# Performance work log

Hardware: AMD Instinct MI355X
Metric: run time of the kernel (lower is better)

The kernel has to match this reference:

```python
import jax, jax.numpy as jnp
import numpy as np

STEPS = 96
H = 4096
I = 1024


def setup_inputs() -> dict:
    key = jax.random.key(0)
    ks = jax.random.split(key, 12)
    kI = 1.0 / np.sqrt(H)  # torch RNN/Linear default init bound
    u = lambda k, shape, b: jax.random.uniform(k, shape, jnp.float32, -b, b)
    return {
        "x": jax.random.normal(ks[0], (1, 1, I), jnp.float32),
        "W_ih0": u(ks[1], (H, I), kI),
        "b_ih0": u(ks[2], (H,), kI),
        "W_hh0": u(ks[3], (H, H), kI),
        "b_hh0": u(ks[4], (H,), kI),
        "W_ih1": u(ks[5], (H, H), kI),
        "b_ih1": u(ks[6], (H,), kI),
        "W_hh1": u(ks[7], (H, H), kI),
        "b_hh1": u(ks[8], (H,), kI),
        "W_fc": u(ks[9], (1, H), kI),
        "b_fc": u(ks[10], (1,), kI),
    }


def reference(x, W_ih0, b_ih0, W_hh0, b_hh0, W_ih1, b_ih1, W_hh1, b_hh1, W_fc, b_fc):
    # x: (1, 1, I) -- seq=batch=1 (the only shapes the torch module accepts).
    xv = x[0, 0]  # (I,) sliding feature window
    h_init = jnp.zeros((2, H), x.dtype)  # num_layers=2 hidden state

    def step(carry, _):
        xw, h = carry
        h0 = jnp.tanh(W_ih0 @ xw + b_ih0 + W_hh0 @ h[0] + b_hh0)
        h1 = jnp.tanh(W_ih1 @ h0 + b_ih1 + W_hh1 @ h[1] + b_hh1)
        y = W_fc @ h1 + b_fc  # (1,) scalar prediction
        xw_new = jnp.concatenate([xw[1:], y])  # shift window, append prediction
        # torch: h0.detach() each outer iteration -> cut grad through carried state
        h_new = jax.lax.stop_gradient(jnp.stack([h0, h1]))
        return (xw_new, h_new), y

    _, ys = jax.lax.scan(step, (xv, h_init), None, length=STEPS)  # ys: (96, 1)
    return ys.reshape(1, STEPS, 1)
```

## Files before the change

kernel.cpp:

```cpp
#include <hip/hip_runtime.h>

#define STEPS 96
#define HDIM 4096
#define IDIM 1024
#define BLOCKS 256
#define THREADS 1024
#define WAVES (THREADS / 64)
#define ROWS_PER_BLOCK (HDIM / BLOCKS)

__device__ inline void wload8(const unsigned short* __restrict__ w, float* o) {
  uint4 u = *reinterpret_cast<const uint4*>(w);
  o[0] = __uint_as_float(u.x << 16);
  o[1] = __uint_as_float(u.x & 0xffff0000u);
  o[2] = __uint_as_float(u.y << 16);
  o[3] = __uint_as_float(u.y & 0xffff0000u);
  o[4] = __uint_as_float(u.z << 16);
  o[5] = __uint_as_float(u.z & 0xffff0000u);
  o[6] = __uint_as_float(u.w << 16);
  o[7] = __uint_as_float(u.w & 0xffff0000u);
}
__device__ inline void wload8(const float* __restrict__ w, float* o) {
  float4 a = *reinterpret_cast<const float4*>(w);
  float4 b = *reinterpret_cast<const float4*>(w + 4);
  o[0] = a.x; o[1] = a.y; o[2] = a.z; o[3] = a.w;
  o[4] = b.x; o[5] = b.y; o[6] = b.z; o[7] = b.w;
}
__device__ inline void wload4(const unsigned short* __restrict__ w, float* o) {
  uint2 u = *reinterpret_cast<const uint2*>(w);
  o[0] = __uint_as_float(u.x << 16);
  o[1] = __uint_as_float(u.x & 0xffff0000u);
  o[2] = __uint_as_float(u.y << 16);
  o[3] = __uint_as_float(u.y & 0xffff0000u);
}
__device__ inline void wload4(const float* __restrict__ w, float* o) {
  float4 f = *reinterpret_cast<const float4*>(w);
  o[0] = f.x; o[1] = f.y; o[2] = f.z; o[3] = f.w;
}

template <typename WT, int NC>
__device__ inline float dot_gh(const WT* __restrict__ w, const float* __restrict__ v, int lane) {
  float acc = 0.f;
#pragma unroll
  for (int it = 0; it < NC / 512; ++it) {
    const int base = it * 512 + lane * 8;
    float wf[8];
    wload8(w + base, wf);
    float4 a = *reinterpret_cast<const float4*>(v + base);
    float4 b = *reinterpret_cast<const float4*>(v + base + 4);
    acc += wf[0] * a.x + wf[1] * a.y + wf[2] * a.z + wf[3] * a.w +
           wf[4] * b.x + wf[5] * b.y + wf[6] * b.z + wf[7] * b.w;
  }
  return acc;
}

template <typename WT>
__device__ inline float dot_win(const WT* __restrict__ w, const float* v, int lane) {
  float acc = 0.f;
#pragma unroll
  for (int it = 0; it < IDIM / 512; ++it) {
    const int base = it * 512 + lane * 8;
    float wf[8];
    wload8(w + base, wf);
#pragma unroll
    for (int k = 0; k < 8; ++k) acc += wf[k] * v[base + k];
  }
  return acc;
}

__device__ inline float wave_reduce(float v) {
#pragma unroll
  for (int off = 32; off > 0; off >>= 1) v += __shfl_xor(v, off);
  return v;
}

template <typename WT>
struct Params {
  const WT *Wih0, *Whh0, *Wih1, *Whh1, *Wfc;
  const float *x, *b_ih0, *b_hh0, *b_ih1, *b_hh1, *b_fc;
  float* h0buf;
  float* h1buf;
  unsigned* leaf;
  unsigned* root;
  unsigned* flag;
  float* out;
};

template <typename WT>
__device__ inline void grid_barrier(const Params<WT>& p, unsigned gen) {
  __syncthreads();
  if (threadIdx.x == 0) {
    __threadfence();
    const int g = blockIdx.x & 7;
    unsigned prev = __hip_atomic_fetch_add(p.leaf + g * 32, 1u, __ATOMIC_RELAXED,
                                           __HIP_MEMORY_SCOPE_AGENT);
    if (prev == gen * (BLOCKS / 8) - 1) {
      unsigned r = __hip_atomic_fetch_add(p.root, 1u, __ATOMIC_RELAXED,
                                          __HIP_MEMORY_SCOPE_AGENT);
      if (r == gen * 8 - 1) {
        __hip_atomic_store(p.flag, gen, __ATOMIC_RELEASE, __HIP_MEMORY_SCOPE_AGENT);
      }
    }
    while (__hip_atomic_load(p.flag, __ATOMIC_RELAXED, __HIP_MEMORY_SCOPE_AGENT) < gen) {
      __builtin_amdgcn_s_sleep(1);
    }
    __threadfence();
  }
  __syncthreads();
}

template <typename WT>
__global__ void __launch_bounds__(THREADS, 4) rnn_kernel(Params<WT> p) {
  __shared__ float win[IDIM + STEPS];
  __shared__ float red[WAVES];

  const int tid = threadIdx.x;
  const int lane = tid & 63;
  const int wv = tid >> 6;
  const int blk = blockIdx.x;
  const int row = blk * ROWS_PER_BLOCK + wv;

  for (int i = tid; i < IDIM; i += THREADS) win[i] = p.x[i];
  __syncthreads();

  unsigned gen = 0;
  for (int t = 0; t < STEPS; ++t) {
    const int par = t & 1;
    float* h0n = p.h0buf + par * HDIM;
    const float* h0o = p.h0buf + (par ^ 1) * HDIM;
    float* h1n = p.h1buf + par * HDIM;
    const float* h1o = p.h1buf + (par ^ 1) * HDIM;

    {
      float acc = dot_win(p.Wih0 + (size_t)row * IDIM, win + t, lane) +
                  dot_gh<WT, HDIM>(p.Whh0 + (size_t)row * HDIM, h0o, lane);
      acc = wave_reduce(acc);
      if (lane == 0) h0n[row] = tanhf(acc + p.b_ih0[row] + p.b_hh0[row]);
    }
    grid_barrier(p, ++gen);

    {
      float acc = dot_gh<WT, HDIM>(p.Wih1 + (size_t)row * HDIM, h0n, lane) +
                  dot_gh<WT, HDIM>(p.Whh1 + (size_t)row * HDIM, h1o, lane);
      acc = wave_reduce(acc);
      if (lane == 0) h1n[row] = tanhf(acc + p.b_ih1[row] + p.b_hh1[row]);
    }
    grid_barrier(p, ++gen);

    {
      const int base = tid * 4;
      float wf[4];
      wload4(p.Wfc + base, wf);
      float4 h = *reinterpret_cast<const float4*>(h1n + base);
      float part = wf[0] * h.x + wf[1] * h.y + wf[2] * h.z + wf[3] * h.w;
      part = wave_reduce(part);
      if (lane == 0) red[wv] = part;
    }
    __syncthreads();
    if (tid == 0) {
      float y = p.b_fc[0];
#pragma unroll
      for (int i = 0; i < WAVES; ++i) y += red[i];
      win[IDIM + t] = y;
      if (blk == 0) p.out[t] = y;
    }
    __syncthreads();
  }
}

__device__ inline unsigned short f2bf(float f) {
  unsigned int u = __float_as_uint(f);
  u += 0x7fffu + ((u >> 16) & 1u);
  return (unsigned short)(u >> 16);
}

__global__ void cvt_kernel(const float* __restrict__ in, unsigned short* __restrict__ out, int n4) {
  int i = blockIdx.x * blockDim.x + threadIdx.x;
  const int stride = gridDim.x * blockDim.x;
  for (; i < n4; i += stride) {
    float4 f = reinterpret_cast<const float4*>(in)[i];
    ushort4 o;
    o.x = f2bf(f.x); o.y = f2bf(f.y); o.z = f2bf(f.z); o.w = f2bf(f.w);
    reinterpret_cast<ushort4*>(out)[i] = o;
  }
}

extern "C" void kernel_launch(void* const* d_in, const int* in_sizes, int n_in,
                              void* d_out, int out_size, void* d_ws, size_t ws_size,
                              hipStream_t stream) {
  const float* x = (const float*)d_in[0];
  const float* Wih0 = (const float*)d_in[1];
  const float* bih0 = (const float*)d_in[2];
  const float* Whh0 = (const float*)d_in[3];
  const float* bhh0 = (const float*)d_in[4];
  const float* Wih1 = (const float*)d_in[5];
  const float* bih1 = (const float*)d_in[6];
  const float* Whh1 = (const float*)d_in[7];
  const float* bhh1 = (const float*)d_in[8];
  const float* Wfc = (const float*)d_in[9];
  const float* bfc = (const float*)d_in[10];
  float* out = (float*)d_out;

  const size_t nIh0 = (size_t)HDIM * IDIM;
  const size_t nHh = (size_t)HDIM * HDIM;
  const size_t nFc = HDIM;
  const size_t bfBytes = (nIh0 + 3 * nHh + nFc) * 2;
  const size_t hFloats = 4 * (size_t)HDIM;
  const size_t barU32 = 8 * 32 + 32 + 32;
  const size_t dynBytes = hFloats * 4 + barU32 * 4;

  if (ws_size >= bfBytes + dynBytes + 256) {
    unsigned short* wih0 = (unsigned short*)d_ws;
    unsigned short* whh0 = wih0 + nIh0;
    unsigned short* wih1 = whh0 + nHh;
    unsigned short* whh1 = wih1 + nHh;
    unsigned short* wfc = whh1 + nHh;
    char* dyn = (char*)d_ws + ((bfBytes + 255) & ~(size_t)255);
    float* hbuf = (float*)dyn;
    unsigned* bar = (unsigned*)(dyn + hFloats * 4);

    cvt_kernel<<<4096, 256, 0, stream>>>(Wih0, wih0, (int)(nIh0 / 4));
    cvt_kernel<<<8192, 256, 0, stream>>>(Whh0, whh0, (int)(nHh / 4));
    cvt_kernel<<<8192, 256, 0, stream>>>(Wih1, wih1, (int)(nHh / 4));
    cvt_kernel<<<8192, 256, 0, stream>>>(Whh1, whh1, (int)(nHh / 4));
    cvt_kernel<<<8, 128, 0, stream>>>(Wfc, wfc, (int)(nFc / 4));
    hipMemsetAsync(dyn, 0, dynBytes, stream);

    Params<unsigned short> p;
    p.Wih0 = wih0; p.Whh0 = whh0; p.Wih1 = wih1; p.Whh1 = whh1; p.Wfc = wfc;
    p.x = x; p.b_ih0 = bih0; p.b_hh0 = bhh0; p.b_ih1 = bih1; p.b_hh1 = bhh1; p.b_fc = bfc;
    p.h0buf = hbuf; p.h1buf = hbuf + 2 * HDIM;
    p.leaf = bar; p.root = bar + 8 * 32; p.flag = bar + 8 * 32 + 32;
    p.out = out;

    void* args[] = {&p};
    hipLaunchCooperativeKernel(reinterpret_cast<void*>(&rnn_kernel<unsigned short>),
                               dim3(BLOCKS), dim3(THREADS), args, 0, stream);
  } else {
    char* dyn = (char*)d_ws;
    float* hbuf = (float*)dyn;
    unsigned* bar = (unsigned*)(dyn + hFloats * 4);
    hipMemsetAsync(dyn, 0, dynBytes, stream);

    Params<float> p;
    p.Wih0 = Wih0; p.Whh0 = Whh0; p.Wih1 = Wih1; p.Whh1 = Whh1; p.Wfc = Wfc;
    p.x = x; p.b_ih0 = bih0; p.b_hh0 = bhh0; p.b_ih1 = bih1; p.b_hh1 = bhh1; p.b_fc = bfc;
    p.h0buf = hbuf; p.h1buf = hbuf + 2 * HDIM;
    p.leaf = bar; p.root = bar + 8 * 32; p.flag = bar + 8 * 32 + 32;
    p.out = out;

    void* args[] = {&p};
    hipLaunchCooperativeKernel(reinterpret_cast<void*>(&rnn_kernel<float>),
                               dim3(BLOCKS), dim3(THREADS), args, 0, stream);
  }
}
```

Baseline: 3.924 ms.

## Keep bf16 weights resident in registers and LDS, reorder recurrence phases

Removes the separate bf16 conversion kernels and instead packs each block's weight rows into bf16 once at kernel start. Whh0, Wih1, Wih0 and Wfc slices are held in registers and the block's Whh1 rows in LDS, so the 96 steps no longer stream weights from HBM/L2. The phases are reordered so that the Whh1·h1 product runs before the barrier, and the Whh0·h0 product for the next step is fused with the Wih1·h0 pass. This reduces per-step memory traffic and keeps two grid barriers per step, with single h buffers. In exchange it uses very high register and LDS pressure (512 threads, 2 rows per wave), which may cause spills or limit occupancy, and it relies on careful ordering so that the single-buffered h0/h1 are safe.

Result: slower. 6.703 ms (+70.8%).

```diff
diff --git a/kernel.cpp b/kernel.cpp
--- a/kernel.cpp
+++ b/kernel.cpp
@@ -4,68 +4,20 @@
 #define HDIM 4096
 #define IDIM 1024
 #define BLOCKS 256
-#define THREADS 1024
-#define WAVES (THREADS / 64)
-#define ROWS_PER_BLOCK (HDIM / BLOCKS)
-
-__device__ inline void wload8(const unsigned short* __restrict__ w, float* o) {
-  uint4 u = *reinterpret_cast<const uint4*>(w);
-  o[0] = __uint_as_float(u.x << 16);
-  o[1] = __uint_as_float(u.x & 0xffff0000u);
-  o[2] = __uint_as_float(u.y << 16);
-  o[3] = __uint_as_float(u.y & 0xffff0000u);
-  o[4] = __uint_as_float(u.z << 16);
-  o[5] = __uint_as_float(u.z & 0xffff0000u);
-  o[6] = __uint_as_float(u.w << 16);
-  o[7] = __uint_as_float(u.w & 0xffff0000u);
-}
-__device__ inline void wload8(const float* __restrict__ w, float* o) {
-  float4 a = *reinterpret_cast<const float4*>(w);
-  float4 b = *reinterpret_cast<const float4*>(w + 4);
-  o[0] = a.x; o[1] = a.y; o[2] = a.z; o[3] = a.w;
-  o[4] = b.x; o[5] = b.y; o[6] = b.z; o[7] = b.w;
-}
-__device__ inline void wload4(const unsigned short* __restrict__ w, float* o) {
-  uint2 u = *reinterpret_cast<const uint2*>(w);
-  o[0] = __uint_as_float(u.x << 16);
-  o[1] = __uint_as_float(u.x & 0xffff0000u);
-  o[2] = __uint_as_float(u.y << 16);
-  o[3] = __uint_as_float(u.y & 0xffff0000u);
-}
-__device__ inline void wload4(const float* __restrict__ w, float* o) {
-  float4 f = *reinterpret_cast<const float4*>(w);
-  o[0] = f.x; o[1] = f.y; o[2] = f.z; o[3] = f.w;
-}
-
-template <typename WT, int NC>
-__device__ inline float dot_gh(const WT* __restrict__ w, const float* __restrict__ v, int lane) {
-  float acc = 0.f;
-#pragma unroll
-  for (int it = 0; it < NC / 512; ++it) {
-    const int base = it * 512 + lane * 8;
-    float wf[8];
-    wload8(w + base, wf);
-    float4 a = *reinterpret_cast<const float4*>(v + base);
-    float4 b = *reinterpret_cast<const float4*>(v + base + 4);
-    acc += wf[0] * a.x + wf[1] * a.y + wf[2] * a.z + wf[3] * a.w +
-           wf[4] * b.x + wf[5] * b.y + wf[6] * b.z + wf[7] * b.w;
-  }
-  return acc;
-}
-
-template <typename WT>
-__device__ inline float dot_win(const WT* __restrict__ w, const float* v, int lane) {
-  float acc = 0.f;
-#pragma unroll
-  for (int it = 0; it < IDIM / 512; ++it) {
-    const int base = it * 512 + lane * 8;
-    float wf[8];
-    wload8(w + base, wf);
-#pragma unroll
-    for (int k = 0; k < 8; ++k) acc += wf[k] * v[base + k];
-  }
-  return acc;
-}
+#define THREADS 512
+#define WAVES 8
+#define ROWS_PER_BLOCK 16
+
+__device__ inline unsigned short f2bf(float f) {
+  unsigned u = __float_as_uint(f);
+  u += 0x7fffu + ((u >> 16) & 1u);
+  return (unsigned short)(u >> 16);
+}
+__device__ inline unsigned pack2(float a, float b) {
+  return (unsigned)f2bf(a) | ((unsigned)f2bf(b) << 16);
+}
+__device__ inline float blo(unsigned p) { return __uint_as_float(p << 16); }
+__device__ inline float bhi(unsigned p) { return __uint_as_float(p & 0xffff0000u); }
 
 __device__ inline float wave_reduce(float v) {
 #pragma unroll
@@ -73,20 +25,14 @@
   return v;
 }
 
-template <typename WT>
 struct Params {
-  const WT *Wih0, *Whh0, *Wih1, *Whh1, *Wfc;
-  const float *x, *b_ih0, *b_hh0, *b_ih1, *b_hh1, *b_fc;
-  float* h0buf;
-  float* h1buf;
-  unsigned* leaf;
-  unsigned* root;
-  unsigned* flag;
-  float* out;
+  const float *x, *Wih0, *bih0, *Whh0, *bhh0, *Wih1, *bih1, *Whh1, *bhh1, *Wfc, *bfc;
+  float *h0, *h1;
+  unsigned *leaf, *root, *flag;
+  float *out;
 };
 
-template <typename WT>
-__device__ inline void grid_barrier(const Params<WT>& p, unsigned gen) {
+__device__ inline void grid_barrier(const Params& p, unsigned gen) {
   __syncthreads();
   if (threadIdx.x == 0) {
     __threadfence();
@@ -108,56 +54,132 @@
   __syncthreads();
 }
 
-template <typename WT>
-__global__ void __launch_bounds__(THREADS, 4) rnn_kernel(Params<WT> p) {
+__global__ void __launch_bounds__(THREADS, 2) rnn_kernel(Params p) {
+  __shared__ unsigned whh1[ROWS_PER_BLOCK * (HDIM / 2)];
   __shared__ float win[IDIM + STEPS];
   __shared__ float red[WAVES];
 
-  const int tid = threadIdx.x;
-  const int lane = tid & 63;
-  const int wv = tid >> 6;
-  const int blk = blockIdx.x;
-  const int row = blk * ROWS_PER_BLOCK + wv;
-
+  const int tid = threadIdx.x, lane = tid & 63, wv = tid >> 6, blk = blockIdx.x;
+  const int r0 = blk * ROWS_PER_BLOCK + wv * 2;
+  const int r1 = r0 + 1;
+
+  for (int rr = 0; rr < ROWS_PER_BLOCK; ++rr) {
+    const float* src = p.Whh1 + (size_t)(blk * ROWS_PER_BLOCK + rr) * HDIM;
+    for (int u = tid; u < HDIM / 2; u += THREADS) {
+      float2 f = *reinterpret_cast<const float2*>(src + 2 * u);
+      whh1[rr * (HDIM / 2) + u] = pack2(f.x, f.y);
+    }
+  }
   for (int i = tid; i < IDIM; i += THREADS) win[i] = p.x[i];
+
+  unsigned wA_ih0[8], wB_ih0[8];
+#pragma unroll
+  for (int j = 0; j < 8; ++j) {
+    const float* s0 = p.Wih0 + (size_t)r0 * IDIM + j * 128 + lane;
+    const float* s1 = p.Wih0 + (size_t)r1 * IDIM + j * 128 + lane;
+    wA_ih0[j] = pack2(s0[0], s0[64]);
+    wB_ih0[j] = pack2(s1[0], s1[64]);
+  }
+  unsigned wA_hh0[32], wB_hh0[32], wA_ih1[32], wB_ih1[32];
+#pragma unroll
+  for (int j = 0; j < 16; ++j) {
+    float4 f;
+    f = *reinterpret_cast<const float4*>(p.Whh0 + (size_t)r0 * HDIM + j * 256 + lane * 4);
+    wA_hh0[2 * j] = pack2(f.x, f.y); wA_hh0[2 * j + 1] = pack2(f.z, f.w);
+    f = *reinterpret_cast<const float4*>(p.Whh0 + (size_t)r1 * HDIM + j * 256 + lane * 4);
+    wB_hh0[2 * j] = pack2(f.x, f.y); wB_hh0[2 * j + 1] = pack2(f.z, f.w);
+    f = *reinterpret_cast<const float4*>(p.Wih1 + (size_t)r0 * HDIM + j * 256 + lane * 4);
+    wA_ih1[2 * j] = pack2(f.x, f.y); wA_ih1[2 * j + 1] = pack2(f.z, f.w);
+    f = *reinterpret_cast<const float4*>(p.Wih1 + (size_t)r1 * HDIM + j * 256 + lane * 4);
+    wB_ih1[2 * j] = pack2(f.x, f.y); wB_ih1[2 * j + 1] = pack2(f.z, f.w);
+  }
+  unsigned wfcp[4];
+  {
+    float4 f = *reinterpret_cast<const float4*>(p.Wfc + tid * 8);
+    wfcp[0] = pack2(f.x, f.y); wfcp[1] = pack2(f.z, f.w);
+    f = *reinterpret_cast<const float4*>(p.Wfc + tid * 8 + 4);
+    wfcp[2] = pack2(f.x, f.y); wfcp[3] = pack2(f.z, f.w);
+  }
+  const float bias0a = p.bih0[r0] + p.bhh0[r0];
+  const float bias0b = p.bih0[r1] + p.bhh0[r1];
+  const float bias1a = p.bih1[r0] + p.bhh1[r0];
+  const float bias1b = p.bih1[r1] + p.bhh1[r1];
+  const float bfc = p.bfc[0];
+
   __syncthreads();
 
+  float p1a = 0.f, p1b = 0.f;
   unsigned gen = 0;
+
   for (int t = 0; t < STEPS; ++t) {
-    const int par = t & 1;
-    float* h0n = p.h0buf + par * HDIM;
-    const float* h0o = p.h0buf + (par ^ 1) * HDIM;
-    float* h1n = p.h1buf + par * HDIM;
-    const float* h1o = p.h1buf + (par ^ 1) * HDIM;
-
+    float a1 = p1a, b1 = p1b;
+#pragma unroll
+    for (int j = 0; j < 8; ++j) {
+      float v0 = win[t + j * 128 + lane];
+      float v1 = win[t + j * 128 + 64 + lane];
+      a1 += v0 * blo(wA_ih0[j]) + v1 * bhi(wA_ih0[j]);
+      b1 += v0 * blo(wB_ih0[j]) + v1 * bhi(wB_ih0[j]);
+    }
+    a1 = wave_reduce(a1);
+    b1 = wave_reduce(b1);
+    if (lane == 0) {
+      p.h0[r0] = tanhf(a1 + bias0a);
+      p.h0[r1] = tanhf(b1 + bias0b);
+    }
+
+    float a2 = 0.f, b2 = 0.f;
     {
-      float acc = dot_win(p.Wih0 + (size_t)row * IDIM, win + t, lane) +
-                  dot_gh<WT, HDIM>(p.Whh0 + (size_t)row * HDIM, h0o, lane);
-      acc = wave_reduce(acc);
-      if (lane == 0) h0n[row] = tanhf(acc + p.b_ih0[row] + p.b_hh0[row]);
-    }
+      const unsigned* wl0 = whh1 + (wv * 2) * (HDIM / 2);
+      const unsigned* wl1 = wl0 + (HDIM / 2);
+#pragma unroll
+      for (int j = 0; j < 16; ++j) {
+        float4 v = *reinterpret_cast<const float4*>(p.h1 + j * 256 + lane * 4);
+        unsigned c0 = wl0[j * 128 + lane * 2], c1 = wl0[j * 128 + lane * 2 + 1];
+        unsigned d0 = wl1[j * 128 + lane * 2], d1 = wl1[j * 128 + lane * 2 + 1];
+        a2 += v.x * blo(c0) + v.y * bhi(c0) + v.z * blo(c1) + v.w * bhi(c1);
+        b2 += v.x * blo(d0) + v.y * bhi(d0) + v.z * blo(d1) + v.w * bhi(d1);
+      }
+    }
+
     grid_barrier(p, ++gen);
 
+    float q1a = 0.f, q1b = 0.f;
+#pragma unroll
+    for (int j = 0; j < 16; ++j) {
+      float4 v = *reinterpret_cast<const float4*>(p.h0 + j * 256 + lane * 4);
+      a2 += v.x * blo(wA_ih1[2 * j]) + v.y * bhi(wA_ih1[2 * j]) +
+            v.z * blo(wA_ih1[2 * j + 1]) + v.w * bhi(wA_ih1[2 * j + 1]);
+      b2 += v.x * blo(wB_ih1[2 * j]) + v.y * bhi(wB_ih1[2 * j]) +
+            v.z * blo(wB_ih1[2 * j + 1]) + v.w * bhi(wB_ih1[2 * j + 1]);
+      q1a += v.x * blo(wA_hh0[2 * j]) + v.y * bhi(wA_hh0[2 * j]) +
+             v.z * blo(wA_hh0[2 * j + 1]) + v.w * bhi(wA_hh0[2 * j + 1]);
+      q1b += v.x * blo(wB_hh0[2 * j]) + v.y * bhi(wB_hh0[2 * j]) +
+             v.z * blo(wB_hh0[2 * j + 1]) + v.w * bhi(wB_hh0[2 * j + 1]);
+    }
+    a2 = wave_reduce(a2);
+    b2 = wave_reduce(b2);
+    if (lane == 0) {
+      p.h1[r0] = tanhf(a2 + bias1a);
+      p.h1[r1] = tanhf(b2 + bias1b);
+    }
+    p1a = q1a;
+    p1b = q1b;
+
+    grid_barrier(p, ++gen);
+
     {
-      float acc = dot_gh<WT, HDIM>(p.Wih1 + (size_t)row * HDIM, h0n, lane) +
-                  dot_gh<WT, HDIM>(p.Whh1 + (size_t)row * HDIM, h1o, lane);
-      acc = wave_reduce(acc);
-      if (lane == 0) h1n[row] = tanhf(acc + p.b_ih1[row] + p.b_hh1[row]);
-    }
-    grid_barrier(p, ++gen);
-
-    {
-      const int base = tid * 4;
-      float wf[4];
-      wload4(p.Wfc + base, wf);
-      float4 h = *reinterpret_cast<const float4*>(h1n + base);
-      float part = wf[0] * h.x + wf[1] * h.y + wf[2] * h.z + wf[3] * h.w;
+      float4 v0 = *reinterpret_cast<const float4*>(p.h1 + tid * 8);
+      float4 v1 = *reinterpret_cast<const float4*>(p.h1 + tid * 8 + 4);
+      float part = v0.x * blo(wfcp[0]) + v0.y * bhi(wfcp[0]) +
+                   v0.z * blo(wfcp[1]) + v0.w * bhi(wfcp[1]) +
+                   v1.x * blo(wfcp[2]) + v1.y * bhi(wfcp[2]) +
+                   v1.z * blo(wfcp[3]) + v1.w * bhi(wfcp[3]);
       part = wave_reduce(part);
       if (lane == 0) red[wv] = part;
     }
     __syncthreads();
     if (tid == 0) {
-      float y = p.b_fc[0];
+      float y = bfc;
 #pragma unroll
       for (int i = 0; i < WAVES; ++i) y += red[i];
       win[IDIM + t] = y;
@@ -167,89 +189,35 @@
   }
 }
 
-__device__ inline unsigned short f2bf(float f) {
-  unsigned int u = __float_as_uint(f);
-  u += 0x7fffu + ((u >> 16) & 1u);
-  return (unsigned short)(u >> 16);
-}
-
-__global__ void cvt_kernel(const float* __restrict__ in, unsigned short* __restrict__ out, int n4) {
-  int i = blockIdx.x * blockDim.x + threadIdx.x;
-  const int stride = gridDim.x * blockDim.x;
-  for (; i < n4; i += stride) {
-    float4 f = reinterpret_cast<const float4*>(in)[i];
-    ushort4 o;
-    o.x = f2bf(f.x); o.y = f2bf(f.y); o.z = f2bf(f.z); o.w = f2bf(f.w);
-    reinterpret_cast<ushort4*>(out)[i] = o;
-  }
-}
-
 extern "C" void kernel_launch(void* const* d_in, const int* in_sizes, int n_in,
                               void* d_out, int out_size, void* d_ws, size_t ws_size,
                               hipStream_t stream) {
-  const float* x = (const float*)d_in[0];
-  const float* Wih0 = (const float*)d_in[1];
-  const float* bih0 = (const float*)d_in[2];
-  const float* Whh0 = (const float*)d_in[3];
-  const float* bhh0 = (const float*)d_in[4];
-  const float* Wih1 = (const float*)d_in[5];
-  const float* bih1 = (const float*)d_in[6];
-  const float* Whh1 = (const float*)d_in[7];
-  const float* bhh1 = (const float*)d_in[8];
-  const float* Wfc = (const float*)d_in[9];
-  const float* bfc = (const float*)d_in[10];
-  float* out = (float*)d_out;
-
-  const size_t nIh0 = (size_t)HDIM * IDIM;
-  const size_t nHh = (size_t)HDIM * HDIM;
-  const size_t nFc = HDIM;
-  const size_t bfBytes = (nIh0 + 3 * nHh + nFc) * 2;
-  const size_t hFloats = 4 * (size_t)HDIM;
-  const size_t barU32 = 8 * 32 + 32 + 32;
-  const size_t dynBytes = hFloats * 4 + barU32 * 4;
-
-  if (ws_size >= bfBytes + dynBytes + 256) {
-    unsigned short* wih0 = (unsigned short*)d_ws;
-    unsigned short* whh0 = wih0 + nIh0;
-    unsigned short* wih1 = whh0 + nHh;
-    unsigned short* whh1 = wih1 + nHh;
-    unsigned short* wfc = whh1 + nHh;
-    char* dyn = (char*)d_ws + ((bfBytes + 255) & ~(size_t)255);
-    float* hbuf = (float*)dyn;
-    unsigned* bar = (unsigned*)(dyn + hFloats * 4);
-
-    cvt_kernel<<<4096, 256, 0, stream>>>(Wih0, wih0, (int)(nIh0 / 4));
-    cvt_kernel<<<8192, 256, 0, stream>>>(Whh0, whh0, (int)(nHh / 4));
-    cvt_kernel<<<8192, 256, 0, stream>>>(Wih1, wih1, (int)(nHh / 4));
-    cvt_kernel<<<8192, 256, 0, stream>>>(Whh1, whh1, (int)(nHh / 4));
-    cvt_kernel<<<8, 128, 0, stream>>>(Wfc, wfc, (int)(nFc / 4));
-    hipMemsetAsync(dyn, 0, dynBytes, stream);
-
-    Params<unsigned short> p;
-    p.Wih0 = wih0; p.Whh0 = whh0; p.Wih1 = wih1; p.Whh1 = whh1; p.Wfc = wfc;
-    p.x = x; p.b_ih0 = bih0; p.b_hh0 = bhh0; p.b_ih1 = bih1; p.b_hh1 = bhh1; p.b_fc = bfc;
-    p.h0buf = hbuf; p.h1buf = hbuf + 2 * HDIM;
-    p.leaf = bar; p.root = bar + 8 * 32; p.flag = bar + 8 * 32 + 32;
-    p.out = out;
-
-    void* args[] = {&p};
-    hipLaunchCooperativeKernel(reinterpret_cast<void*>(&rnn_kernel<unsigned short>),
-                               dim3(BLOCKS), dim3(THREADS), args, 0, stream);
-  } else {
-    char* dyn = (char*)d_ws;
-    float* hbuf = (float*)dyn;
-    unsigned* bar = (unsigned*)(dyn + hFloats * 4);
-    hipMemsetAsync(dyn, 0, dynBytes, stream);
-
-    Params<float> p;
-    p.Wih0 = Wih0; p.Whh0 = Whh0; p.Wih1 = Wih1; p.Whh1 = Whh1; p.Wfc = Wfc;
-    p.x = x; p.b_ih0 = bih0; p.b_hh0 = bhh0; p.b_ih1 = bih1; p.b_hh1 = bhh1; p.b_fc = bfc;
-    p.h0buf = hbuf; p.h1buf = hbuf + 2 * HDIM;
-    p.leaf = bar; p.root = bar + 8 * 32; p.flag = bar + 8 * 32 + 32;
-    p.out = out;
-
-    void* args[] = {&p};
-    hipLaunchCooperativeKernel(reinterpret_cast<void*>(&rnn_kernel<float>),
-                               dim3(BLOCKS), dim3(THREADS), args, 0, stream);
-  }
-}
+  Params p;
+  p.x = (const float*)d_in[0];
+  p.Wih0 = (const float*)d_in[1];
+  p.bih0 = (const float*)d_in[2];
+  p.Whh0 = (const float*)d_in[3];
+  p.bhh0 = (const float*)d_in[4];
+  p.Wih1 = (const float*)d_in[5];
+  p.bih1 = (const float*)d_in[6];
+  p.Whh1 = (const float*)d_in[7];
+  p.bhh1 = (const float*)d_in[8];
+  p.Wfc = (const float*)d_in[9];
+  p.bfc = (const float*)d_in[10];
+  p.out = (float*)d_out;
+
+  float* hbuf = (float*)d_ws;
+  p.h0 = hbuf;
+  p.h1 = hbuf + HDIM;
+  unsigned* bar = (unsigned*)(hbuf + 2 * HDIM);
+  p.leaf = bar;
+  p.root = bar + 8 * 32;
+  p.flag = bar + 8 * 32 + 32;
+
+  const size_t dynBytes = 2 * HDIM * sizeof(float) + (8 * 32 + 64) * sizeof(unsigned);
+  hipMemsetAsync(d_ws, 0, dynBytes, stream);
+
+  void* args[] = {&p};
+  hipLaunchCooperativeKernel(reinterpret_cast<void*>(&rnn_kernel),
+                             dim3(BLOCKS), dim3(THREADS), args, 0, stream);
+}
```
